# Kernel tuning notes

Hardware: AMD Instinct MI355X
Metric: run time of the kernel (lower is better)

## Reference

```python
import jax, jax.numpy as jnp
import numpy as np

TOPK = 2  # config.expert_topk


def setup_inputs() -> dict:
    key = jax.random.key(0)
    k1, k2, k3, k4 = jax.random.split(key, 4)
    B, T, D, H, E = 2, 2048, 768, 3072, 8
    x = jax.random.normal(k1, (B, T, D), jnp.float32)
    gate_w = jax.random.normal(k2, (E, D), jnp.float32) * 0.02   # nn.Linear(D, E).weight
    w_fc = jax.random.normal(k3, (E, H, D), jnp.float32) * 0.02  # per-expert c_fc.weight [out,in]
    w_proj = jax.random.normal(k4, (E, D, H), jnp.float32) * 0.02  # per-expert c_proj.weight
    return {"x": x, "gate_w": gate_w, "w_fc": w_fc, "w_proj": w_proj}


def reference(x, gate_w, w_fc, w_proj):
    # x: [B,T,D]; gate_w: [E,D]; w_fc: [E,H,D]; w_proj: [E,D,H]
    B, T, D = x.shape
    E = gate_w.shape[0]
    N = B * T
    xf = x.reshape(N, D)

    gate_logits = xf @ gate_w.T                       # [N,E]
    gate_probs = jax.nn.softmax(gate_logits, axis=-1)
    rw, idx = jax.lax.top_k(gate_probs, TOPK)          # [N,k]
    rw = rw / jnp.sum(rw, axis=-1, keepdims=True)

    # combine[n,e] = sum_k rw[n,k] * (idx[n,k]==e); zero for unselected experts,
    # so the dense per-expert MLP below computes the same math as torch dispatch.
    oh = jax.nn.one_hot(idx, E, dtype=xf.dtype)        # [N,k,E]
    combine = jnp.einsum('nk,nke->ne', rw, oh)         # [N,E]

    h = jnp.einsum('nd,ehd->neh', xf, w_fc)            # [N,E,H]
    h = jnp.square(jax.nn.relu(h))                     # relu(x)^2
    y = jnp.einsum('neh,edh->ned', h, w_proj)          # [N,E,D]
    out = jnp.einsum('ned,ne->nd', y, combine).reshape(B, T, D)

    # expert_freq = bincount(expert_indices)/N, detached in the loss
    counts = jnp.sum(oh, axis=(0, 1))                  # [E]
    expert_freq = counts / N
    balance_loss = jnp.sum(gate_probs.mean(axis=0) * jax.lax.stop_gradient(expert_freq)) * E
    return out, balance_loss
```

## Files before the change

### kernel.cpp

```cpp
#include <hip/hip_runtime.h>
#include <hip/hip_bf16.h>

typedef __bf16 bf16_t;
typedef bf16_t bf16x8 __attribute__((ext_vector_type(8)));
typedef bf16_t bf16x4 __attribute__((ext_vector_type(4)));
typedef float f32x4 __attribute__((ext_vector_type(4)));

#define N_TOK 4096
#define DIM   768
#define HID   3072
#define NEXP  8
#define PADROWS 9216
#define MMAX  32

#define OFF_COUNTS 0
#define OFF_PSUM   32
#define OFF_OFFPAD 64
#define OFF_CURSOR 128
#define OFF_TOKE   256
#define OFF_TOKW   (OFF_TOKE + 4*8192)
#define OFF_PERMT  (OFF_TOKW + 4*8192)
#define OFF_PERMW  (OFF_PERMT + 4*PADROWS)
#define OFF_XP     (((OFF_PERMW + 4*PADROWS) + 511) & ~511ull)
#define OFF_WFC    (OFF_XP + 2ull*PADROWS*DIM)
#define OFF_WPJ    (OFF_WFC + 2ull*NEXP*HID*DIM)
#define OFF_H      (OFF_WPJ + 2ull*NEXP*DIM*HID)
#define WS_NEEDED  (OFF_H + 2ull*PADROWS*HID)

#define GATE_BLOCKS (N_TOK / 4)
#define CONVH_BLOCKS 4608
#define GEMM1_BLOCKS (8 * 24 * MMAX)

__device__ __forceinline__ void async_copy16(const bf16_t* g, bf16_t* l) {
    __builtin_amdgcn_global_load_lds(
        (const __attribute__((address_space(1))) void*)g,
        (__attribute__((address_space(3))) void*)l, 16, 0, 0);
}

__device__ __forceinline__ void convert_chunk(const float* __restrict__ src,
                                              bf16_t* __restrict__ dst,
                                              int cid, int t) {
    const long long base = (long long)cid * 256 + t;
    const long long stride = (long long)CONVH_BLOCKS * 256;
#pragma unroll
    for (int it = 0; it < 4; it++) {
        const long long i4 = base + (long long)it * stride;
        f32x4 v = __builtin_nontemporal_load(((const f32x4*)src) + i4);
        bf16x4 o;
        o[0] = (bf16_t)v.x; o[1] = (bf16_t)v.y;
        o[2] = (bf16_t)v.z; o[3] = (bf16_t)v.w;
        *(bf16x4*)(dst + i4 * 4) = o;
    }
}

__global__ __launch_bounds__(256) void prep_kernel(
    const float* __restrict__ w_fc, bf16_t* __restrict__ wfc_b,
    const float* __restrict__ x, const float* __restrict__ gw,
    int* __restrict__ cs_part, float* __restrict__ ps_part,
    int* __restrict__ tok_e, float* __restrict__ tok_w)
{
    __shared__ float ps[8];
    __shared__ int cs[8];

    if (blockIdx.x >= GATE_BLOCKS) {
        convert_chunk(w_fc, wfc_b, blockIdx.x - GATE_BLOCKS, threadIdx.x);
        return;
    }

    if (threadIdx.x < 8) { ps[threadIdx.x] = 0.f; cs[threadIdx.x] = 0; }
    __syncthreads();

    const int bid = blockIdx.x;
    const int wv = threadIdx.x >> 6, lane = threadIdx.x & 63;
    const int n = bid * 4 + wv;

    float acc[8];
#pragma unroll
    for (int e = 0; e < 8; e++) acc[e] = 0.f;
    const float* xr = x + (size_t)n * DIM;
#pragma unroll
    for (int c = 0; c < 12; c++) {
        const float xv = xr[c * 64 + lane];
#pragma unroll
        for (int e = 0; e < 8; e++) acc[e] += xv * gw[e * DIM + c * 64 + lane];
    }
#pragma unroll
    for (int e = 0; e < 8; e++)
        for (int off = 32; off > 0; off >>= 1) acc[e] += __shfl_xor(acc[e], off, 64);

    float mx = acc[0];
#pragma unroll
    for (int e = 1; e < 8; e++) mx = fmaxf(mx, acc[e]);
    float p[8], s = 0.f;
#pragma unroll
    for (int e = 0; e < 8; e++) { p[e] = expf(acc[e] - mx); s += p[e]; }

    int e1 = 0;
#pragma unroll
    for (int e = 1; e < 8; e++) if (p[e] > p[e1]) e1 = e;
    int e2 = (e1 == 0) ? 1 : 0;
#pragma unroll
    for (int e = 0; e < 8; e++) if (e != e1 && p[e] > p[e2]) e2 = e;
    const float denom = p[e1] + p[e2];

    if (lane == 0) {
        tok_e[2 * n] = e1; tok_e[2 * n + 1] = e2;
        tok_w[2 * n] = p[e1] / denom; tok_w[2 * n + 1] = p[e2] / denom;
        const float inv = 1.f / s;
#pragma unroll
        for (int e = 0; e < 8; e++) atomicAdd(&ps[e], p[e] * inv);
        atomicAdd(&cs[e1], 1); atomicAdd(&cs[e2], 1);
    }
    __syncthreads();
    if (threadIdx.x < 8) {
        ps_part[bid * 8 + threadIdx.x] = ps[threadIdx.x];
        cs_part[bid * 8 + threadIdx.x] = cs[threadIdx.x];
    }
}

__global__ __launch_bounds__(256) void finalize_scatter(
    const int* cs_part, const float* ps_part,
    const int* __restrict__ tok_e, const float* __restrict__ tok_w,
    int* __restrict__ counts, int* __restrict__ off_pad,
    int* perm_tok, int* inv_pos, float* __restrict__ out_loss)
{
    __shared__ float rps[256];
    __shared__ int rcs[256];
    __shared__ int s_cur[8];
    const int t = threadIdx.x;
    const int e = t & 7, chunk = t >> 3;
    float psum = 0.f; int csum = 0;
#pragma unroll
    for (int i = 0; i < 32; i++) {
        const int b = chunk * 32 + i;
        psum += ps_part[b * 8 + e];
        csum += cs_part[b * 8 + e];
    }
    rps[t] = psum; rcs[t] = csum;
    __syncthreads();
    for (int s = 128; s >= 8; s >>= 1) {
        if (t < s) { rps[t] += rps[t + s]; rcs[t] += rcs[t + s]; }
        __syncthreads();
    }
    if (t == 0) {
        int off = 0; float loss = 0.f;
        for (int k = 0; k < 8; k++) {
            counts[k] = rcs[k];
            off_pad[k] = off; s_cur[k] = off;
            off += ((rcs[k] + 127) & ~127);
            loss += rps[k] * (float)rcs[k];
        }
        off_pad[8] = off;
        *out_loss = loss * 8.f / ((float)N_TOK * (float)N_TOK);
    }
    __syncthreads();
    for (int r = 0; r < N_TOK / 256; r++) {
        const int n = r * 256 + t;
#pragma unroll
        for (int k = 0; k < 2; k++) {
            const int ee = tok_e[2 * n + k];
            const int pos = atomicAdd(&s_cur[ee], 1);
            perm_tok[pos] = n;
            inv_pos[2 * n + k] = pos;
        }
    }
}

__global__ __launch_bounds__(256) void gather_x_kernel(
    const float* __restrict__ x, const int* __restrict__ off_pad,
    const int* __restrict__ counts, const int* __restrict__ perm_tok,
    bf16_t* __restrict__ xp)
{
    __shared__ int so[9], scnt[8];
    if (threadIdx.x < 9) so[threadIdx.x] = off_pad[threadIdx.x];
    if (threadIdx.x < 8) scnt[threadIdx.x] = counts[threadIdx.x];
    __syncthreads();
    const int gid = blockIdx.x * 256 + threadIdx.x;
    const int p = gid / 192;
    const int c = (gid - p * 192) * 4;
    int e = 0;
#pragma unroll
    for (int k = 1; k < 8; k++) if (p >= so[k]) e = k;
    const bool valid = (p < so[8]) && (p - so[e] < scnt[e]);
    float4 v = make_float4(0.f, 0.f, 0.f, 0.f);
    if (valid) {
        const int tok = perm_tok[p];
        v = *(const float4*)(x + (size_t)tok * DIM + c);
    }
    bf16x4 o; o[0] = (bf16_t)v.x; o[1] = (bf16_t)v.y; o[2] = (bf16_t)v.z; o[3] = (bf16_t)v.w;
    *(bf16x4*)(xp + (size_t)p * DIM + c) = o;
}

__global__ __launch_bounds__(256, 4) void gemm1_kernel(
    const bf16_t* __restrict__ xp, const bf16_t* __restrict__ wfc,
    const int* __restrict__ off_pad, bf16_t* __restrict__ h,
    const float* __restrict__ w_proj, bf16_t* __restrict__ wpj_b)
{
    const int id = blockIdx.x;
    if (id >= GEMM1_BLOCKS) {
        convert_chunk(w_proj, wpj_b, id - GEMM1_BLOCKS, threadIdx.x);
        return;
    }
    const int e = id & 7;
    const int slot = id >> 3;
    const int n_t = slot / MMAX, m_t = slot % MMAX;

    const int seg0 = off_pad[e];
    const int cnt_pad = off_pad[e + 1] - seg0;
    const int m0 = m_t * 128;
    if (m0 >= cnt_pad) return;
    const int n0 = n_t * 128;

    __shared__ bf16_t As[128 * 64];
    __shared__ bf16_t Bs[128 * 64];

    const int t = threadIdx.x;
    const int srow = t >> 3, sc = t & 7;
    const int gsc = sc ^ (srow & 7);
    const bf16_t* abase = xp + (size_t)(seg0 + m0 + srow) * DIM + gsc * 8;
    const bf16_t* bbase = wfc + ((size_t)e * HID + n0 + srow) * DIM + gsc * 8;

    const int wv = t >> 6, lane = t & 63;
    const int lrow = lane & 15, quad = lane >> 4;
    const int wm = (wv & 1) * 64, wn = (wv >> 1) * 64;
    const int sw = lrow & 7;

    f32x4 acc[4][4] = {};

    for (int k0 = 0; k0 < DIM; k0 += 64) {
        __syncthreads();
#pragma unroll
        for (int ii = 0; ii < 4; ii++) {
            async_copy16(abase + (size_t)ii * 32 * DIM + k0, &As[(ii * 256 + t) * 8]);
            async_copy16(bbase + (size_t)ii * 32 * DIM + k0, &Bs[(ii * 256 + t) * 8]);
        }
        __syncthreads();
#pragma unroll
        for (int kh = 0; kh < 2; kh++) {
            const int ch = ((kh * 4 + quad) ^ sw) * 8;
            bf16x8 af[4], bfv[4];
#pragma unroll
            for (int i = 0; i < 4; i++)
                af[i] = *(bf16x8*)&As[(wm + i * 16 + lrow) * 64 + ch];
#pragma unroll
            for (int j = 0; j < 4; j++)
                bfv[j] = *(bf16x8*)&Bs[(wn + j * 16 + lrow) * 64 + ch];
#pragma unroll
            for (int i = 0; i < 4; i++)
#pragma unroll
                for (int j = 0; j < 4; j++)
                    acc[i][j] = __builtin_amdgcn_mfma_f32_16x16x32_bf16(af[i], bfv[j], acc[i][j], 0, 0, 0);
        }
    }

#pragma unroll
    for (int i = 0; i < 4; i++) {
#pragma unroll
        for (int g = 0; g < 4; g++) {
            const int m = m0 + wm + i * 16 + quad * 4 + g;
            bf16_t* hrow = h + (size_t)(seg0 + m) * HID + n0 + wn + lrow;
#pragma unroll
            for (int j = 0; j < 4; j++) {
                float v = fmaxf(acc[i][j][g], 0.f);
                hrow[j * 16] = (bf16_t)(v * v);
            }
        }
    }
}

__global__ __launch_bounds__(256, 4) void gemm2_kernel(
    const bf16_t* __restrict__ h, const bf16_t* __restrict__ wpj,
    const int* __restrict__ off_pad, const int* __restrict__ counts,
    bf16_t* __restrict__ y0, bf16_t* __restrict__ y1)
{
    const int id = blockIdx.x;
    const int e = id & 7;
    const int slot = id >> 3;
    const int split = slot / (MMAX * 6);
    const int rem = slot % (MMAX * 6);
    const int m_t = rem / 6, n_t = rem % 6;

    const int seg0 = off_pad[e];
    const int cnt = counts[e];
    const int m0 = m_t * 128;
    if (m0 >= cnt) return;
    const int n0 = n_t * 128;
    const int kbeg = split * (HID / 2);

    __shared__ bf16_t As[128 * 64];
    __shared__ bf16_t Bs[128 * 64];

    const int t = threadIdx.x;
    const int srow = t >> 3, sc = t & 7;
    const int gsc = sc ^ (srow & 7);
    const bf16_t* abase = h + (size_t)(seg0 + m0 + srow) * HID + kbeg + gsc * 8;
    const bf16_t* bbase = wpj + ((size_t)e * DIM + n0 + srow) * HID + kbeg + gsc * 8;

    const int wv = t >> 6, lane = t & 63;
    const int lrow = lane & 15, quad = lane >> 4;
    const int wm = (wv & 1) * 64, wn = (wv >> 1) * 64;
    const int sw = lrow & 7;

    f32x4 acc[4][4] = {};

    for (int k0 = 0; k0 < HID / 2; k0 += 64) {
        __syncthreads();
#pragma unroll
        for (int ii = 0; ii < 4; ii++) {
            async_copy16(abase + (size_t)ii * 32 * HID + k0, &As[(ii * 256 + t) * 8]);
            async_copy16(bbase + (size_t)ii * 32 * HID + k0, &Bs[(ii * 256 + t) * 8]);
        }
        __syncthreads();
#pragma unroll
        for (int kh = 0; kh < 2; kh++) {
            const int ch = ((kh * 4 + quad) ^ sw) * 8;
            bf16x8 af[4], bfv[4];
#pragma unroll
            for (int i = 0; i < 4; i++)
                af[i] = *(bf16x8*)&As[(wm + i * 16 + lrow) * 64 + ch];
#pragma unroll
            for (int j = 0; j < 4; j++)
                bfv[j] = *(bf16x8*)&Bs[(wn + j * 16 + lrow) * 64 + ch];
#pragma unroll
            for (int i = 0; i < 4; i++)
#pragma unroll
                for (int j = 0; j < 4; j++)
                    acc[i][j] = __builtin_amdgcn_mfma_f32_16x16x32_bf16(af[i], bfv[j], acc[i][j], 0, 0, 0);
        }
    }

    bf16_t* yout = split ? y1 : y0;
#pragma unroll
    for (int i = 0; i < 4; i++) {
#pragma unroll
        for (int g = 0; g < 4; g++) {
            const int m = m0 + wm + i * 16 + quad * 4 + g;
            if (m < cnt) {
                bf16_t* yrow = yout + (size_t)(seg0 + m) * DIM + n0 + wn + lrow;
#pragma unroll
                for (int j = 0; j < 4; j++)
                    yrow[j * 16] = (bf16_t)acc[i][j][g];
            }
        }
    }
}

__global__ __launch_bounds__(192) void combine_kernel(
    const bf16_t* __restrict__ y0, const bf16_t* __restrict__ y1,
    const int* __restrict__ inv_pos, const float* __restrict__ tok_w,
    float* __restrict__ out)
{
    const int n = blockIdx.x;
    const int d = threadIdx.x * 4;
    const int p1 = inv_pos[2 * n], p2 = inv_pos[2 * n + 1];
    const float w1 = tok_w[2 * n], w2 = tok_w[2 * n + 1];
    bf16x4 a0 = *(const bf16x4*)(y0 + (size_t)p1 * DIM + d);
    bf16x4 a1 = *(const bf16x4*)(y1 + (size_t)p1 * DIM + d);
    bf16x4 b0 = *(const bf16x4*)(y0 + (size_t)p2 * DIM + d);
    bf16x4 b1 = *(const bf16x4*)(y1 + (size_t)p2 * DIM + d);
    float4 o;
    o.x = w1 * ((float)a0[0] + (float)a1[0]) + w2 * ((float)b0[0] + (float)b1[0]);
    o.y = w1 * ((float)a0[1] + (float)a1[1]) + w2 * ((float)b0[1] + (float)b1[1]);
    o.z = w1 * ((float)a0[2] + (float)a1[2]) + w2 * ((float)b0[2] + (float)b1[2]);
    o.w = w1 * ((float)a0[3] + (float)a1[3]) + w2 * ((float)b0[3] + (float)b1[3]);
    *(float4*)(out + (size_t)n * DIM + d) = o;
}

extern "C" void kernel_launch(void* const* d_in, const int* in_sizes, int n_in,
                              void* d_out, int out_size, void* d_ws, size_t ws_size,
                              hipStream_t stream) {
    const float* x      = (const float*)d_in[0];
    const float* gate_w = (const float*)d_in[1];
    const float* w_fc   = (const float*)d_in[2];
    const float* w_proj = (const float*)d_in[3];
    float* out = (float*)d_out;

    if (ws_size < WS_NEEDED) return;

    char* w = (char*)d_ws;
    int*    counts    = (int*)(w + OFF_COUNTS);
    int*    off_pad   = (int*)(w + OFF_OFFPAD);
    int*    tok_e     = (int*)(w + OFF_TOKE);
    float*  tok_w     = (float*)(w + OFF_TOKW);
    int*    perm_tok  = (int*)(w + OFF_PERMT);
    int*    inv_pos   = (int*)(w + OFF_PERMW);
    bf16_t* xp        = (bf16_t*)(w + OFF_XP);
    bf16_t* wfc_b     = (bf16_t*)(w + OFF_WFC);
    bf16_t* wpj_b     = (bf16_t*)(w + OFF_WPJ);
    bf16_t* hbuf      = (bf16_t*)(w + OFF_H);

    int*   cs_part = perm_tok;
    float* ps_part = (float*)inv_pos;
    bf16_t* y0 = xp;
    bf16_t* y1 = wfc_b;

    prep_kernel<<<GATE_BLOCKS + CONVH_BLOCKS, 256, 0, stream>>>(
        w_fc, wfc_b, x, gate_w, cs_part, ps_part, tok_e, tok_w);
    finalize_scatter<<<1, 256, 0, stream>>>(cs_part, ps_part, tok_e, tok_w,
                                            counts, off_pad, perm_tok, inv_pos,
                                            out + (size_t)out_size - 1);
    gather_x_kernel<<<PADROWS * DIM / 4 / 256, 256, 0, stream>>>(x, off_pad, counts, perm_tok, xp);

    gemm1_kernel<<<GEMM1_BLOCKS + CONVH_BLOCKS, 256, 0, stream>>>(
        xp, wfc_b, off_pad, hbuf, w_proj, wpj_b);
    gemm2_kernel<<<8 * 2 * MMAX * 6, 256, 0, stream>>>(hbuf, wpj_b, off_pad, counts, y0, y1);
    combine_kernel<<<N_TOK, 192, 0, stream>>>(y0, y1, inv_pos, tok_w, out);
}
```

Measured before the change: 297.9 us.

## Double-buffer gemm1 LDS tiles and move w_fc conversion into gather kernel

Gemm1 now uses two LDS buffers so the async global-to-LDS copy of the next K-slice is issued before the MFMAs on the current slice, cutting one barrier per iteration and overlapping load latency with compute. Launch bounds drop from 4 to 2 blocks per SM because LDS use per block doubles. The w_fc fp32-to-bf16 conversion moves out of the gate kernel and into the gather kernel, so the small gate pass and the single-block finalize no longer wait behind the large conversion. Occupancy falls, and the single barrier per iteration relies on global_load_lds completion ordering at the barrier.

```diff
diff --git a/kernel.cpp b/kernel.cpp
--- a/kernel.cpp
+++ b/kernel.cpp
@@ -29,6 +29,7 @@
 
 #define GATE_BLOCKS (N_TOK / 4)
 #define CONVH_BLOCKS 4608
+#define GATHER_BLOCKS (PADROWS * DIM / 4 / 256)
 #define GEMM1_BLOCKS (8 * 24 * MMAX)
 
 __device__ __forceinline__ void async_copy16(const bf16_t* g, bf16_t* l) {
@@ -53,20 +54,13 @@
     }
 }
 
-__global__ __launch_bounds__(256) void prep_kernel(
-    const float* __restrict__ w_fc, bf16_t* __restrict__ wfc_b,
+__global__ __launch_bounds__(256) void gate_kernel(
     const float* __restrict__ x, const float* __restrict__ gw,
     int* __restrict__ cs_part, float* __restrict__ ps_part,
     int* __restrict__ tok_e, float* __restrict__ tok_w)
 {
     __shared__ float ps[8];
     __shared__ int cs[8];
-
-    if (blockIdx.x >= GATE_BLOCKS) {
-        convert_chunk(w_fc, wfc_b, blockIdx.x - GATE_BLOCKS, threadIdx.x);
-        return;
-    }
-
     if (threadIdx.x < 8) { ps[threadIdx.x] = 0.f; cs[threadIdx.x] = 0; }
     __syncthreads();
 
@@ -169,8 +163,13 @@
 __global__ __launch_bounds__(256) void gather_x_kernel(
     const float* __restrict__ x, const int* __restrict__ off_pad,
     const int* __restrict__ counts, const int* __restrict__ perm_tok,
-    bf16_t* __restrict__ xp)
-{
+    bf16_t* __restrict__ xp,
+    const float* __restrict__ w_fc, bf16_t* __restrict__ wfc_b)
+{
+    if (blockIdx.x >= GATHER_BLOCKS) {
+        convert_chunk(w_fc, wfc_b, blockIdx.x - GATHER_BLOCKS, threadIdx.x);
+        return;
+    }
     __shared__ int so[9], scnt[8];
     if (threadIdx.x < 9) so[threadIdx.x] = off_pad[threadIdx.x];
     if (threadIdx.x < 8) scnt[threadIdx.x] = counts[threadIdx.x];
@@ -191,7 +190,7 @@
     *(bf16x4*)(xp + (size_t)p * DIM + c) = o;
 }
 
-__global__ __launch_bounds__(256, 4) void gemm1_kernel(
+__global__ __launch_bounds__(256, 2) void gemm1_kernel(
     const bf16_t* __restrict__ xp, const bf16_t* __restrict__ wfc,
     const int* __restrict__ off_pad, bf16_t* __restrict__ h,
     const float* __restrict__ w_proj, bf16_t* __restrict__ wpj_b)
@@ -211,8 +210,8 @@
     if (m0 >= cnt_pad) return;
     const int n0 = n_t * 128;
 
-    __shared__ bf16_t As[128 * 64];
-    __shared__ bf16_t Bs[128 * 64];
+    __shared__ bf16_t As[2][128 * 64];
+    __shared__ bf16_t Bs[2][128 * 64];
 
     const int t = threadIdx.x;
     const int srow = t >> 3, sc = t & 7;
@@ -227,30 +226,42 @@
 
     f32x4 acc[4][4] = {};
 
-    for (int k0 = 0; k0 < DIM; k0 += 64) {
-        __syncthreads();
-#pragma unroll
-        for (int ii = 0; ii < 4; ii++) {
-            async_copy16(abase + (size_t)ii * 32 * DIM + k0, &As[(ii * 256 + t) * 8]);
-            async_copy16(bbase + (size_t)ii * 32 * DIM + k0, &Bs[(ii * 256 + t) * 8]);
-        }
-        __syncthreads();
+#pragma unroll
+    for (int ii = 0; ii < 4; ii++) {
+        async_copy16(abase + (size_t)ii * 32 * DIM, &As[0][(ii * 256 + t) * 8]);
+        async_copy16(bbase + (size_t)ii * 32 * DIM, &Bs[0][(ii * 256 + t) * 8]);
+    }
+    __syncthreads();
+
+    for (int ks = 0; ks < DIM / 64; ks++) {
+        const int cur = ks & 1;
+        if (ks + 1 < DIM / 64) {
+            const int k0n = (ks + 1) * 64;
+#pragma unroll
+            for (int ii = 0; ii < 4; ii++) {
+                async_copy16(abase + (size_t)ii * 32 * DIM + k0n, &As[cur ^ 1][(ii * 256 + t) * 8]);
+                async_copy16(bbase + (size_t)ii * 32 * DIM + k0n, &Bs[cur ^ 1][(ii * 256 + t) * 8]);
+            }
+        }
+        const bf16_t* Ac = As[cur];
+        const bf16_t* Bc = Bs[cur];
 #pragma unroll
         for (int kh = 0; kh < 2; kh++) {
             const int ch = ((kh * 4 + quad) ^ sw) * 8;
             bf16x8 af[4], bfv[4];
 #pragma unroll
             for (int i = 0; i < 4; i++)
-                af[i] = *(bf16x8*)&As[(wm + i * 16 + lrow) * 64 + ch];
+                af[i] = *(bf16x8*)&Ac[(wm + i * 16 + lrow) * 64 + ch];
 #pragma unroll
             for (int j = 0; j < 4; j++)
-                bfv[j] = *(bf16x8*)&Bs[(wn + j * 16 + lrow) * 64 + ch];
+                bfv[j] = *(bf16x8*)&Bc[(wn + j * 16 + lrow) * 64 + ch];
 #pragma unroll
             for (int i = 0; i < 4; i++)
 #pragma unroll
                 for (int j = 0; j < 4; j++)
                     acc[i][j] = __builtin_amdgcn_mfma_f32_16x16x32_bf16(af[i], bfv[j], acc[i][j], 0, 0, 0);
         }
+        __syncthreads();
     }
 
 #pragma unroll
@@ -394,12 +405,12 @@
     bf16_t* y0 = xp;
     bf16_t* y1 = wfc_b;
 
-    prep_kernel<<<GATE_BLOCKS + CONVH_BLOCKS, 256, 0, stream>>>(
-        w_fc, wfc_b, x, gate_w, cs_part, ps_part, tok_e, tok_w);
+    gate_kernel<<<GATE_BLOCKS, 256, 0, stream>>>(x, gate_w, cs_part, ps_part, tok_e, tok_w);
     finalize_scatter<<<1, 256, 0, stream>>>(cs_part, ps_part, tok_e, tok_w,
                                             counts, off_pad, perm_tok, inv_pos,
                                             out + (size_t)out_size - 1);
-    gather_x_kernel<<<PADROWS * DIM / 4 / 256, 256, 0, stream>>>(x, off_pad, counts, perm_tok, xp);
+    gather_x_kernel<<<GATHER_BLOCKS + CONVH_BLOCKS, 256, 0, stream>>>(
+        x, off_pad, counts, perm_tok, xp, w_fc, wfc_b);
 
     gemm1_kernel<<<GEMM1_BLOCKS + CONVH_BLOCKS, 256, 0, stream>>>(
         xp, wfc_b, off_pad, hbuf, w_proj, wpj_b);
```

After: 313.0 us. 5.1% more time.
